# Kernel optimization log

Hardware: AMD Instinct MI355X
Metric: run time of the kernel (lower is better)

Reference implementation:

```python
import jax, jax.numpy as jnp
import numpy as np

DEPTH = 6
N_EST = 16
IN_DIM = 512
N_CLASSES = 100
BATCH = 8192
N_NODES = 2 ** DEPTH - 1   # 63 internal nodes
N_LEAVES = 2 ** DEPTH      # 64 leaves


def entmax15(t):
    # Source's (nonstandard) entmax15: softmax(relu(t)**1.5)
    z = jax.nn.relu(t)
    return jax.nn.softmax(z ** 1.5, axis=-1)


def _leaf_paths():
    # Ancestor node index and branch bit for every (depth level j, leaf l),
    # exactly matching: idx = 2**(j-1) + l // 2**(depth-(j-1)) - 1
    #                   bit = (l // 2**(depth-j)) % 2
    l = np.arange(N_LEAVES)
    j = np.arange(1, DEPTH + 1)[:, None]
    idx = (2 ** (j - 1) + l[None, :] // (2 ** (DEPTH - (j - 1))) - 1).astype(np.int32)
    bits = ((l[None, :] // (2 ** (DEPTH - j))) % 2).astype(np.int32)
    return jnp.asarray(idx), jnp.asarray(bits)  # both (DEPTH, N_LEAVES)


def setup_inputs() -> dict:
    key = jax.random.key(0)
    kx, kT, kL = jax.random.split(key, 3)
    x = jax.random.normal(kx, (BATCH, IN_DIM), dtype=jnp.float32)
    T = jax.random.normal(kT, (N_EST, N_NODES, IN_DIM), dtype=jnp.float32)
    L = jax.random.normal(kL, (N_EST, N_LEAVES, N_CLASSES), dtype=jnp.float32)
    return {"x": x, "T": T, "L": L}


def reference(x, T, L):
    # Hard feature selection with straight-through: forward = hardmax(entmax15(T)),
    # backward = 0 (in the torch source, I = I - (I - hardmax(I)) kills the gradient).
    I_soft = entmax15(T)  # (E, N, D)
    I = jax.lax.stop_gradient(
        (I_soft == I_soft.max(axis=-1, keepdims=True)).astype(x.dtype)
    )
    # Per-node split decisions for all nodes at once.
    t_dot = jnp.einsum('end,end->en', T, I)          # (E, N) threshold value
    x_dot = jnp.einsum('bd,end->ben', x, I)          # (B, E, N) selected feature
    # s = s - (s - floor(s)) == floor(s); floor has zero gradient (matches torch).
    s = jnp.floor(t_dot[None, :, :] - x_dot)         # (B, E, N)

    idx, bits = _leaf_paths()                        # (DEPTH, N_LEAVES)
    sg = s[..., idx]                                 # (B, E, DEPTH, N_LEAVES)
    factors = jnp.where(bits[None, None] == 1, 1.0 - sg, sg)
    p = jnp.prod(factors, axis=2)                    # (B, E, N_LEAVES)

    # Leaf values, summed over the ensemble.
    y_hat = jnp.einsum('bel,elc->bc', p, L)          # (B, C)
    return jax.nn.softmax(y_hat, axis=-1)
```

## Files before the change

### kernel.cpp

```cpp
#include <hip/hip_runtime.h>
#include <hip/hip_bf16.h>
#include <math.h>

#define IN_DIM 512
#define NC 100
#define NN 63
#define NE 16
#define BATCH 8192
#define XP 516

typedef __attribute__((ext_vector_type(8))) short bf16x8;
typedef __attribute__((ext_vector_type(4))) float f32x4;

static __device__ __forceinline__ ushort bf16_bits(__hip_bfloat16 h) {
  union { __hip_bfloat16 b; ushort u; } cv; cv.b = h; return cv.u;
}

__global__ __launch_bounds__(64) void node_argmax_kernel(
    const float* __restrict__ T, float* __restrict__ tmax, int* __restrict__ dstar) {
  const int node = blockIdx.x;
  const float4* row = reinterpret_cast<const float4*>(T + (size_t)node * IN_DIM);
  const int lane = threadIdx.x;
  float best = -INFINITY;
  int bidx = 0;
#pragma unroll
  for (int i = 0; i < 2; ++i) {
    const int f4 = lane + 64 * i;
    const float4 v = row[f4];
    const int base = f4 * 4;
    if (v.x > best) { best = v.x; bidx = base; }
    if (v.y > best) { best = v.y; bidx = base + 1; }
    if (v.z > best) { best = v.z; bidx = base + 2; }
    if (v.w > best) { best = v.w; bidx = base + 3; }
  }
#pragma unroll
  for (int off = 32; off; off >>= 1) {
    const float ov = __shfl_xor(best, off);
    const int oi = __shfl_xor(bidx, off);
    if (ov > best || (ov == best && oi < bidx)) { best = ov; bidx = oi; }
  }
  if (lane == 0) {
    tmax[node] = best;
    dstar[node] = bidx;
  }
}

__global__ __launch_bounds__(256) void lt_frag_kernel(const float* __restrict__ L,
                                                      ushort* __restrict__ Bfrag) {
  const int i = blockIdx.x * 256 + threadIdx.x;
  const int j = i & 7;
  const int lane = (i >> 3) & 63;
  const int cf = (i >> 9) & 7;
  const int hl = (i >> 12) & 1;
  const int kc = i >> 13;
  const int k = kc * 32 + (lane >> 4) * 8 + j;
  const int c = cf * 16 + (lane & 15);
  const float val = (c < NC) ? L[(size_t)k * NC + c] : 0.0f;
  const __hip_bfloat16 hb = __float2bfloat16(val);
  ushort outv;
  if (hl == 0) {
    outv = bf16_bits(hb);
  } else {
    const __hip_bfloat16 lb = __float2bfloat16(val - __bfloat162float(hb));
    outv = bf16_bits(lb);
  }
  Bfrag[i] = outv;
}

__global__ __launch_bounds__(256) void forest_fused_kernel(
    const float* __restrict__ x, const ushort* __restrict__ Bfrag,
    const float* __restrict__ tmaxg, const int* __restrict__ dstarg,
    float* __restrict__ out) {
  __shared__ __align__(16) float xl[16 * XP];
  __shared__ float tl[NE * NN];
  __shared__ int dl[NE * NN];
  __shared__ __align__(16) float red[4 * 16 * 128];
  const int tid = threadIdx.x;
  const int b0 = blockIdx.x * 16;
  const int w = tid >> 6, lane = tid & 63;

  {
    const float4* xg = reinterpret_cast<const float4*>(x + (size_t)b0 * IN_DIM);
#pragma unroll
    for (int i = 0; i < 8; ++i) {
      const int idx = tid + i * 256;
      const int r = idx >> 7, c4 = idx & 127;
      *reinterpret_cast<float4*>(&xl[r * XP + c4 * 4]) = xg[r * 128 + c4];
    }
    for (int i = tid; i < NE * NN; i += 256) { tl[i] = tmaxg[i]; dl[i] = dstarg[i]; }
  }
  __syncthreads();

  const int r = lane & 15;
  const int lgq = lane >> 4;
  const float* xr = &xl[r * XP];
  const bf16x8* bf = reinterpret_cast<const bf16x8*>(Bfrag);

  f32x4 acc[8];
#pragma unroll
  for (int cf = 0; cf < 8; ++cf) acc[cf] = (f32x4)0.0f;

  for (int t = 0; t < 8; ++t) {
    const int kc = w * 8 + t;
    const int e = kc >> 1;
    const int lg = (kc & 1) * 4 + lgq;
    const float* te = &tl[e * NN];
    const int* de = &dl[e * NN];

    const float s1 = floorf(te[0] - xr[de[0]]);
    const int n2 = 1 + (lg >> 2), n3 = 3 + (lg >> 1), n4 = 7 + lg;
    const float s2 = floorf(te[n2] - xr[de[n2]]);
    const float s3 = floorf(te[n3] - xr[de[n3]]);
    const float s4 = floorf(te[n4] - xr[de[n4]]);
    const int n5 = 15 + 2 * lg, n6 = 31 + 4 * lg;
    const float s5a = floorf(te[n5] - xr[de[n5]]);
    const float s5b = floorf(te[n5 + 1] - xr[de[n5 + 1]]);
    const float s60 = floorf(te[n6] - xr[de[n6]]);
    const float s61 = floorf(te[n6 + 1] - xr[de[n6 + 1]]);
    const float s62 = floorf(te[n6 + 2] - xr[de[n6 + 2]]);
    const float s63 = floorf(te[n6 + 3] - xr[de[n6 + 3]]);

    const float f1 = ((lg >> 2) & 1) ? 1.0f - s1 : s1;
    const float f2 = ((lg >> 1) & 1) ? 1.0f - s2 : s2;
    const float f3 = (lg & 1) ? 1.0f - s3 : s3;
    const float stem = f1 * f2 * f3;
    const float qa = stem * s4, qb = stem * (1.0f - s4);
    const float w00 = qa * s5a, w01 = qa * (1.0f - s5a);
    const float w10 = qb * s5b, w11 = qb * (1.0f - s5b);
    float p[8];
    p[0] = w00 * s60; p[1] = w00 * (1.0f - s60);
    p[2] = w01 * s61; p[3] = w01 * (1.0f - s61);
    p[4] = w10 * s62; p[5] = w10 * (1.0f - s62);
    p[6] = w11 * s63; p[7] = w11 * (1.0f - s63);

    union { ushort u[8]; bf16x8 v; } H, Lo;
#pragma unroll
    for (int i2 = 0; i2 < 8; ++i2) {
      const __hip_bfloat16 hb = __float2bfloat16(p[i2]);
      const float hf = __bfloat162float(hb);
      H.u[i2] = bf16_bits(hb);
      Lo.u[i2] = bf16_bits(__float2bfloat16(p[i2] - hf));
    }
    const bf16x8 Ah = H.v, Al = Lo.v;

    const size_t bbase = (size_t)kc * 1024;
#pragma unroll
    for (int cf = 0; cf < 8; ++cf) {
      const bf16x8 bh = bf[bbase + (size_t)cf * 64 + lane];
      const bf16x8 bl = bf[bbase + 512 + (size_t)cf * 64 + lane];
      acc[cf] = __builtin_amdgcn_mfma_f32_16x16x32_bf16(Ah, bh, acc[cf], 0, 0, 0);
      acc[cf] = __builtin_amdgcn_mfma_f32_16x16x32_bf16(Al, bh, acc[cf], 0, 0, 0);
      acc[cf] = __builtin_amdgcn_mfma_f32_16x16x32_bf16(Ah, bl, acc[cf], 0, 0, 0);
      acc[cf] = __builtin_amdgcn_mfma_f32_16x16x32_bf16(Al, bl, acc[cf], 0, 0, 0);
    }
  }

  {
    const int rlo = (lane >> 4) * 4;
    const int cl = lane & 15;
#pragma unroll
    for (int cf = 0; cf < 8; ++cf)
#pragma unroll
      for (int jj = 0; jj < 4; ++jj)
        red[(w * 16 + rlo + jj) * 128 + cf * 16 + cl] = acc[cf][jj];
  }
  __syncthreads();

  const int rr = tid >> 4;
  const int cg = tid & 15;
  float v[8];
#pragma unroll
  for (int j = 0; j < 8; ++j) {
    const int c = cg * 8 + j;
    v[j] = red[(0 * 16 + rr) * 128 + c] + red[(1 * 16 + rr) * 128 + c] +
           red[(2 * 16 + rr) * 128 + c] + red[(3 * 16 + rr) * 128 + c];
  }
  float m = -INFINITY;
#pragma unroll
  for (int j = 0; j < 8; ++j)
    if (cg * 8 + j < NC) m = fmaxf(m, v[j]);
#pragma unroll
  for (int off = 1; off < 16; off <<= 1) m = fmaxf(m, __shfl_xor(m, off));
  float ev[8];
  float ss = 0.0f;
#pragma unroll
  for (int j = 0; j < 8; ++j) {
    ev[j] = (cg * 8 + j < NC) ? __expf(v[j] - m) : 0.0f;
    ss += ev[j];
  }
#pragma unroll
  for (int off = 1; off < 16; off <<= 1) ss += __shfl_xor(ss, off);
  const float inv = 1.0f / ss;
  float* orow = out + (size_t)(b0 + rr) * NC + cg * 8;
  if (cg < 12) {
    *reinterpret_cast<float4*>(orow) =
        make_float4(ev[0] * inv, ev[1] * inv, ev[2] * inv, ev[3] * inv);
    *reinterpret_cast<float4*>(orow + 4) =
        make_float4(ev[4] * inv, ev[5] * inv, ev[6] * inv, ev[7] * inv);
  } else if (cg == 12) {
    *reinterpret_cast<float4*>(orow) =
        make_float4(ev[0] * inv, ev[1] * inv, ev[2] * inv, ev[3] * inv);
  }
}

extern "C" void kernel_launch(void* const* d_in, const int* in_sizes, int n_in,
                              void* d_out, int out_size, void* d_ws, size_t ws_size,
                              hipStream_t stream) {
  const float* x = (const float*)d_in[0];
  const float* T = (const float*)d_in[1];
  const float* L = (const float*)d_in[2];
  float* out = (float*)d_out;

  char* ws = (char*)d_ws;
  ushort* Bfrag = (ushort*)ws;
  float* tmax = (float*)(ws + 524288);
  int* dstar = (int*)(ws + 528384);

  node_argmax_kernel<<<NE * NN, 64, 0, stream>>>(T, tmax, dstar);
  lt_frag_kernel<<<1024, 256, 0, stream>>>(L, Bfrag);
  forest_fused_kernel<<<BATCH / 16, 256, 0, stream>>>(x, Bfrag, tmax, dstar, out);
}
```

Before: 26.07 us.

## Merge argmax and L-fragment prep kernels; prefetch B fragments before split compute

Combines the node-argmax and leaf-table fragment conversion into one prep kernel, removing one launch and its serialization gap. In the main kernel, all 16 B-fragment loads for a k-chunk are issued before the split-decision arithmetic, so their global latency overlaps the floor/product computation. Adds launch_bounds(256,2) to cap registers for two blocks per CU, but the extra register arrays could cause spills.

```diff
diff --git a/kernel.cpp b/kernel.cpp
--- a/kernel.cpp
+++ b/kernel.cpp
@@ -16,58 +16,62 @@
   union { __hip_bfloat16 b; ushort u; } cv; cv.b = h; return cv.u;
 }
 
-__global__ __launch_bounds__(64) void node_argmax_kernel(
-    const float* __restrict__ T, float* __restrict__ tmax, int* __restrict__ dstar) {
-  const int node = blockIdx.x;
-  const float4* row = reinterpret_cast<const float4*>(T + (size_t)node * IN_DIM);
-  const int lane = threadIdx.x;
-  float best = -INFINITY;
-  int bidx = 0;
-#pragma unroll
-  for (int i = 0; i < 2; ++i) {
-    const int f4 = lane + 64 * i;
-    const float4 v = row[f4];
-    const int base = f4 * 4;
-    if (v.x > best) { best = v.x; bidx = base; }
-    if (v.y > best) { best = v.y; bidx = base + 1; }
-    if (v.z > best) { best = v.z; bidx = base + 2; }
-    if (v.w > best) { best = v.w; bidx = base + 3; }
-  }
-#pragma unroll
-  for (int off = 32; off; off >>= 1) {
-    const float ov = __shfl_xor(best, off);
-    const int oi = __shfl_xor(bidx, off);
-    if (ov > best || (ov == best && oi < bidx)) { best = ov; bidx = oi; }
-  }
-  if (lane == 0) {
-    tmax[node] = best;
-    dstar[node] = bidx;
-  }
-}
-
-__global__ __launch_bounds__(256) void lt_frag_kernel(const float* __restrict__ L,
-                                                      ushort* __restrict__ Bfrag) {
-  const int i = blockIdx.x * 256 + threadIdx.x;
-  const int j = i & 7;
-  const int lane = (i >> 3) & 63;
-  const int cf = (i >> 9) & 7;
-  const int hl = (i >> 12) & 1;
-  const int kc = i >> 13;
-  const int k = kc * 32 + (lane >> 4) * 8 + j;
-  const int c = cf * 16 + (lane & 15);
-  const float val = (c < NC) ? L[(size_t)k * NC + c] : 0.0f;
-  const __hip_bfloat16 hb = __float2bfloat16(val);
-  ushort outv;
-  if (hl == 0) {
-    outv = bf16_bits(hb);
-  } else {
-    const __hip_bfloat16 lb = __float2bfloat16(val - __bfloat162float(hb));
-    outv = bf16_bits(lb);
-  }
-  Bfrag[i] = outv;
-}
-
-__global__ __launch_bounds__(256) void forest_fused_kernel(
+__global__ __launch_bounds__(256) void prep_kernel(
+    const float* __restrict__ T, const float* __restrict__ L,
+    ushort* __restrict__ Bfrag, float* __restrict__ tmax, int* __restrict__ dstar) {
+  const int tid = threadIdx.x;
+  const int bid = blockIdx.x;
+
+  {
+    const int i = bid * 256 + tid;
+    const int j = i & 7;
+    const int lane = (i >> 3) & 63;
+    const int cf = (i >> 9) & 7;
+    const int hl = (i >> 12) & 1;
+    const int kc = i >> 13;
+    const int k = kc * 32 + (lane >> 4) * 8 + j;
+    const int c = cf * 16 + (lane & 15);
+    const float val = (c < NC) ? L[(size_t)k * NC + c] : 0.0f;
+    const __hip_bfloat16 hb = __float2bfloat16(val);
+    ushort outv;
+    if (hl == 0) {
+      outv = bf16_bits(hb);
+    } else {
+      const __hip_bfloat16 lb = __float2bfloat16(val - __bfloat162float(hb));
+      outv = bf16_bits(lb);
+    }
+    Bfrag[i] = outv;
+  }
+
+  if (bid < NE * NN && tid < 64) {
+    const float4* row = reinterpret_cast<const float4*>(T + (size_t)bid * IN_DIM);
+    const int lane = tid;
+    float best = -INFINITY;
+    int bidx = 0;
+#pragma unroll
+    for (int i = 0; i < 2; ++i) {
+      const int f4 = lane + 64 * i;
+      const float4 v = row[f4];
+      const int base = f4 * 4;
+      if (v.x > best) { best = v.x; bidx = base; }
+      if (v.y > best) { best = v.y; bidx = base + 1; }
+      if (v.z > best) { best = v.z; bidx = base + 2; }
+      if (v.w > best) { best = v.w; bidx = base + 3; }
+    }
+#pragma unroll
+    for (int off = 32; off; off >>= 1) {
+      const float ov = __shfl_xor(best, off);
+      const int oi = __shfl_xor(bidx, off);
+      if (ov > best || (ov == best && oi < bidx)) { best = ov; bidx = oi; }
+    }
+    if (lane == 0) {
+      tmax[bid] = best;
+      dstar[bid] = bidx;
+    }
+  }
+}
+
+__global__ __launch_bounds__(256, 2) void forest_fused_kernel(
     const float* __restrict__ x, const ushort* __restrict__ Bfrag,
     const float* __restrict__ tmaxg, const int* __restrict__ dstarg,
     float* __restrict__ out) {
@@ -104,9 +108,17 @@
     const int kc = w * 8 + t;
     const int e = kc >> 1;
     const int lg = (kc & 1) * 4 + lgq;
+
+    const size_t bbase = (size_t)kc * 1024;
+    bf16x8 BH[8], BL[8];
+#pragma unroll
+    for (int cf = 0; cf < 8; ++cf) {
+      BH[cf] = bf[bbase + (size_t)cf * 64 + lane];
+      BL[cf] = bf[bbase + 512 + (size_t)cf * 64 + lane];
+    }
+
     const float* te = &tl[e * NN];
     const int* de = &dl[e * NN];
-
     const float s1 = floorf(te[0] - xr[de[0]]);
     const int n2 = 1 + (lg >> 2), n3 = 3 + (lg >> 1), n4 = 7 + lg;
     const float s2 = floorf(te[n2] - xr[de[n2]]);
@@ -143,15 +155,12 @@
     }
     const bf16x8 Ah = H.v, Al = Lo.v;
 
-    const size_t bbase = (size_t)kc * 1024;
 #pragma unroll
     for (int cf = 0; cf < 8; ++cf) {
-      const bf16x8 bh = bf[bbase + (size_t)cf * 64 + lane];
-      const bf16x8 bl = bf[bbase + 512 + (size_t)cf * 64 + lane];
-      acc[cf] = __builtin_amdgcn_mfma_f32_16x16x32_bf16(Ah, bh, acc[cf], 0, 0, 0);
-      acc[cf] = __builtin_amdgcn_mfma_f32_16x16x32_bf16(Al, bh, acc[cf], 0, 0, 0);
-      acc[cf] = __builtin_amdgcn_mfma_f32_16x16x32_bf16(Ah, bl, acc[cf], 0, 0, 0);
-      acc[cf] = __builtin_amdgcn_mfma_f32_16x16x32_bf16(Al, bl, acc[cf], 0, 0, 0);
+      acc[cf] = __builtin_amdgcn_mfma_f32_16x16x32_bf16(Ah, BH[cf], acc[cf], 0, 0, 0);
+      acc[cf] = __builtin_amdgcn_mfma_f32_16x16x32_bf16(Al, BH[cf], acc[cf], 0, 0, 0);
+      acc[cf] = __builtin_amdgcn_mfma_f32_16x16x32_bf16(Ah, BL[cf], acc[cf], 0, 0, 0);
+      acc[cf] = __builtin_amdgcn_mfma_f32_16x16x32_bf16(Al, BL[cf], acc[cf], 0, 0, 0);
     }
   }
 
@@ -216,7 +225,6 @@
   float* tmax = (float*)(ws + 524288);
   int* dstar = (int*)(ws + 528384);
 
-  node_argmax_kernel<<<NE * NN, 64, 0, stream>>>(T, tmax, dstar);
-  lt_frag_kernel<<<1024, 256, 0, stream>>>(L, Bfrag);
+  prep_kernel<<<1024, 256, 0, stream>>>(T, L, Bfrag, tmax, dstar);
   forest_fused_kernel<<<BATCH / 16, 256, 0, stream>>>(x, Bfrag, tmax, dstar, out);
 }
```

Measured after the change: 23.98 us. 8.0% less time.
